# Performance work log

Measured on AMD Instinct MI355X. Metric: run time of the kernel, lower is better.

## Reference

```python
import jax, jax.numpy as jnp
import numpy as np

B, C, H, W = 8, 256, 128, 128
SH, SW = 8, 8            # stoken_size
HH, WW = H // SH, W // SW
NH = 8                   # num_heads
HD = C // NH             # head_dim = 32
KD = HD                  # key_dim (attn_ratio=1)
ATTN_SCALE = KD ** (-0.5)
AFF_SCALE = C ** (-0.5)


def unfold9(x):
    """x: (B,C,hh,ww) -> (B, hh*ww, C, 9); matches Unfold(3) + transpose/reshape."""
    b, c, hh, ww = x.shape
    xp = jnp.pad(x, ((0, 0), (0, 0), (1, 1), (1, 1)))
    p = jnp.stack([xp[:, :, dy:dy + hh, dx:dx + ww]
                   for dy in range(3) for dx in range(3)], axis=2)  # (B,C,9,hh,ww)
    return p.transpose(0, 3, 4, 1, 2).reshape(b, hh * ww, c, 9)


def fold9(y):
    """y: (B,C,9,hh,ww) -> (B,C,hh,ww); matches Fold(3) (conv_transpose with identity kernels)."""
    hh, ww = y.shape[-2:]
    yp = jnp.pad(y, ((0, 0), (0, 0), (0, 0), (1, 1), (1, 1)))
    out = 0.
    for dy in range(3):
        for dx in range(3):
            out = out + yp[:, :, dy * 3 + dx, 2 - dy:2 - dy + hh, 2 - dx:2 - dx + ww]
    return out


def attention(sf, w_qkv, w_pe, w_proj):
    """Attention module with attn_ratio=1 (Conv layers have act=False, BN identity)."""
    b, c, hh, ww = sf.shape
    n = hh * ww
    qkv = jnp.einsum('oc,bchw->bohw', w_qkv, sf).reshape(b, NH, 2 * KD + HD, n)
    q, k, v = jnp.split(qkv, [KD, 2 * KD], axis=2)
    attn = jax.nn.softmax(jnp.einsum('bhkn,bhkm->bhnm', q, k) * ATTN_SCALE, axis=-1)
    o = jnp.einsum('bhdm,bhnm->bhdn', v, attn).reshape(b, c, hh, ww)
    pe = jax.lax.conv_general_dilated(
        v.reshape(b, c, hh, ww), w_pe, (1, 1), ((1, 1), (1, 1)),
        dimension_numbers=('NCHW', 'OIHW', 'NCHW'), feature_group_count=c)
    return jnp.einsum('oc,bchw->bohw', w_proj, o + pe)


def setup_inputs() -> dict:
    key = jax.random.key(0)
    k0, k1, k2, k3 = jax.random.split(key, 4)
    x = jax.random.normal(k0, (B, C, H, W), dtype=jnp.float32)
    w_qkv = jax.random.normal(k1, (3 * C, C), dtype=jnp.float32) * 0.05
    w_pe = jax.random.normal(k2, (C, 1, 3, 3), dtype=jnp.float32) * 0.05
    w_proj = jax.random.normal(k3, (C, C), dtype=jnp.float32) * 0.05
    return {'x': x, 'w_qkv': w_qkv, 'w_pe': w_pe, 'w_proj': w_proj}


def reference(x, w_qkv, w_pe, w_proj):
    # H,W divisible by stoken_size -> no padding branch
    xb = x.reshape(B, C, HH, SH, WW, SW)
    stoken = xb.mean(axis=(3, 5))                                   # (B,C,hh,ww) adaptive_avg_pool2d
    pix = xb.transpose(0, 2, 4, 3, 5, 1).reshape(B, HH * WW, SH * SW, C)
    # --- single no-grad iteration (n_iter=1) ---
    sf9 = unfold9(stoken)                                            # (B,n,C,9)
    aff = jax.nn.softmax(jnp.einsum('bnpc,bnck->bnpk', pix, sf9) * AFF_SCALE, axis=-1)
    aff = jax.lax.stop_gradient(aff)                                 # torch.no_grad
    asum = aff.sum(axis=2).transpose(0, 2, 1).reshape(B, 1, 9, HH, WW)
    asum = jax.lax.stop_gradient(fold9(asum))                        # (B,1,hh,ww)
    # --- super-token aggregation ---
    sf = jnp.einsum('bnpc,bnpk->bnck', pix, aff)                     # (B,n,C,9)
    sf = fold9(sf.transpose(0, 2, 3, 1).reshape(B, C, 9, HH, WW))    # (B,C,hh,ww)
    sf = sf / (asum + 1e-12)
    # --- refine with attention ---
    sf = attention(sf, w_qkv, w_pe, w_proj)
    # --- scatter back to pixels ---
    sf9b = unfold9(sf)                                               # (B,n,C,9)
    pix_out = jnp.einsum('bnck,bnpk->bnpc', sf9b, aff)               # (B,n,h*w,C)
    return pix_out.reshape(B, HH, WW, C, SH, SW).transpose(0, 3, 1, 4, 2, 5).reshape(B, C, H, W)
```

## Files before the change

### kernel.cpp

```cpp
#include <hip/hip_runtime.h>
#include <cstdint>
#include <cstddef>


#define AFF_SCALE 0.0625f
#define ATTN_SCALE 0.17677669529663687f

__device__ __forceinline__ float dpp_add_xor1(float v) {
    int p = __builtin_amdgcn_update_dpp(0, __float_as_int(v), 0xB1, 0xF, 0xF, true);
    return v + __int_as_float(p);
}
__device__ __forceinline__ float dpp_add_xor2(float v) {
    int p = __builtin_amdgcn_update_dpp(0, __float_as_int(v), 0x4E, 0xF, 0xF, true);
    return v + __int_as_float(p);
}

__global__ __launch_bounds__(128) void stoken_kernel(
    const float* __restrict__ x, float* __restrict__ stok_pad)
{
    int blk = blockIdx.x;
    int i  = blk & 15;
    int bc = blk >> 4;
    int t  = threadIdx.x;
    const float* xr = x + ((size_t)bc * 128 + i * 8) * 128 + t;
    float s = 0.f;
#pragma unroll
    for (int r = 0; r < 8; ++r) s += xr[r * 128];
    s += __shfl_down(s, 4, 64);
    s += __shfl_down(s, 2, 64);
    s += __shfl_down(s, 1, 64);
    if ((t & 7) == 0) {
        int j = t >> 3;
        int b = bc >> 8, c = bc & 255;
        stok_pad[(((size_t)b * 18 + (i + 1)) * 18 + (j + 1)) * 256 + c] =
            s * (1.f / 64.f);
    }
}

__global__ __launch_bounds__(256, 4) void aff_kernel(
    const float* __restrict__ x, const float* __restrict__ stok_pad,
    float* __restrict__ aff_g, float* __restrict__ asum_g)
{
    __shared__ __align__(16) float sfs[9 * 260];
    __shared__ __align__(16) float part[576];

    int bid  = blockIdx.x;
    int xcd  = bid & 7, slot_ = bid >> 3;
    int pair = xcd * 128 + (slot_ >> 1);
    int m = pair & 7, i = (pair >> 3) & 15, b = pair >> 7;
    int j = m * 2 + (slot_ & 1);
    int bn = b * 256 + i * 16 + j;
    int t = threadIdx.x;

    {
        const float* spT = stok_pad + (size_t)b * 324 * 256;
#pragma unroll
        for (int dy = 0; dy < 3; ++dy)
#pragma unroll
            for (int dx = 0; dx < 3; ++dx) {
                int r = i + dy, cn = j + dx;
                float v = 0.f;
                if ((unsigned)(r - 1) < 16u && (unsigned)(cn - 1) < 16u)
                    v = spT[((size_t)r * 18 + cn) * 256 + t];
                sfs[(dy * 3 + dx) * 260 + t] = v;
            }
    }
    part[t] = 0.f;
    part[t + 256] = 0.f;
    if (t < 64) part[t + 512] = 0.f;
    __syncthreads();

    int w = t >> 6, l = t & 63;
    {
        int pq = l >> 2, cgl = l & 3;
        int cbase = w * 64 + cgl * 16;
        int pi = pq >> 1, pj4 = (pq & 1) * 4;
        const float* xb = x + (size_t)(b * 256) * 16384
                            + (size_t)(i * 8 + pi) * 128 + j * 8 + pj4;
        float acc[4][9];
#pragma unroll
        for (int ii = 0; ii < 4; ++ii)
#pragma unroll
            for (int k = 0; k < 9; ++k) acc[ii][k] = 0.f;

#pragma unroll
        for (int c4i = 0; c4i < 4; ++c4i) {
            int c = cbase + c4i * 4;
            const float4 p0 = *(const float4*)&xb[(size_t)(c + 0) * 16384];
            const float4 p1 = *(const float4*)&xb[(size_t)(c + 1) * 16384];
            const float4 p2 = *(const float4*)&xb[(size_t)(c + 2) * 16384];
            const float4 p3 = *(const float4*)&xb[(size_t)(c + 3) * 16384];
#pragma unroll
            for (int k = 0; k < 9; ++k) {
                const float4 sv = *(const float4*)&sfs[k * 260 + c];
                acc[0][k] += p0.x * sv.x + p1.x * sv.y + p2.x * sv.z + p3.x * sv.w;
                acc[1][k] += p0.y * sv.x + p1.y * sv.y + p2.y * sv.z + p3.y * sv.w;
                acc[2][k] += p0.z * sv.x + p1.z * sv.y + p2.z * sv.z + p3.z * sv.w;
                acc[3][k] += p0.w * sv.x + p1.w * sv.y + p2.w * sv.z + p3.w * sv.w;
            }
        }
#pragma unroll
        for (int ii = 0; ii < 4; ++ii)
#pragma unroll
            for (int k = 0; k < 9; ++k) {
                acc[ii][k] = dpp_add_xor1(acc[ii][k]);
                acc[ii][k] = dpp_add_xor2(acc[ii][k]);
            }
#pragma unroll
        for (int k = 0; k < 9; ++k) {
            float v01 = (cgl & 1) ? acc[1][k] : acc[0][k];
            float v23 = (cgl & 1) ? acc[3][k] : acc[2][k];
            float vk  = (cgl & 2) ? v23 : v01;
            atomicAdd(&part[l * 9 + k], vk);
        }
    }
    __syncthreads();

    if (t < 64) {
        float a[9];
        float mx = -1e30f;
#pragma unroll
        for (int k = 0; k < 9; ++k) {
            float v = part[t * 9 + k] * AFF_SCALE;
            a[k] = v;
            mx = fmaxf(mx, v);
        }
        float ssum = 0.f;
#pragma unroll
        for (int k = 0; k < 9; ++k) { a[k] = __expf(a[k] - mx); ssum += a[k]; }
        float inv = 1.f / ssum;
#pragma unroll
        for (int k = 0; k < 9; ++k) {
            a[k] *= inv;
            aff_g[(size_t)bn * 576 + k * 64 + t] = a[k];
        }
#pragma unroll
        for (int k = 0; k < 9; ++k) {
            float r = a[k];
            r += __shfl_down(r, 32, 64); r += __shfl_down(r, 16, 64);
            r += __shfl_down(r, 8, 64);  r += __shfl_down(r, 4, 64);
            r += __shfl_down(r, 2, 64);  r += __shfl_down(r, 1, 64);
            if (t == 0) asum_g[(size_t)bn * 9 + k] = r;
        }
    }
}

__global__ __launch_bounds__(256, 4) void agg_kernel(
    const float* __restrict__ x, const float* __restrict__ aff_g,
    float* __restrict__ agg)
{
    __shared__ __align__(16) float affs[9 * 64];

    int bid  = blockIdx.x;
    int xcd  = bid & 7, slot_ = bid >> 3;
    int pair = xcd * 128 + (slot_ >> 1);
    int m = pair & 7, i = (pair >> 3) & 15, b = pair >> 7;
    int j = m * 2 + (slot_ & 1);
    int bn = b * 256 + i * 16 + j;
    int t = threadIdx.x;

    {
        const float* ag = aff_g + (size_t)bn * 576;
        affs[t] = ag[t];
        affs[t + 256] = ag[t + 256];
        if (t < 64) affs[t + 512] = ag[t + 512];
    }
    __syncthreads();

    int w = t >> 6, l = t & 63;
    int cql = l >> 2, pq2 = l & 3;
    int cb2 = w * 64 + cql * 4;
    const float* xb = x + (size_t)(b * 256) * 16384 + (size_t)(i * 8) * 128 + j * 8;
    float acc2[4][9];
#pragma unroll
    for (int ii = 0; ii < 4; ++ii)
#pragma unroll
        for (int k = 0; k < 9; ++k) acc2[ii][k] = 0.f;

#pragma unroll
    for (int pp = 0; pp < 4; ++pp) {
        int p4 = pq2 * 4 + pp;
        int pi = p4 >> 1, pj4 = (p4 & 1) * 4;
        const float* xr = xb + (size_t)pi * 128 + pj4;
        const float4 q0 = *(const float4*)&xr[(size_t)(cb2 + 0) * 16384];
        const float4 q1 = *(const float4*)&xr[(size_t)(cb2 + 1) * 16384];
        const float4 q2 = *(const float4*)&xr[(size_t)(cb2 + 2) * 16384];
        const float4 q3 = *(const float4*)&xr[(size_t)(cb2 + 3) * 16384];
#pragma unroll
        for (int k = 0; k < 9; ++k) {
            const float4 av = *(const float4*)&affs[k * 64 + p4 * 4];
            acc2[0][k] += q0.x * av.x + q0.y * av.y + q0.z * av.z + q0.w * av.w;
            acc2[1][k] += q1.x * av.x + q1.y * av.y + q1.z * av.z + q1.w * av.w;
            acc2[2][k] += q2.x * av.x + q2.y * av.y + q2.z * av.z + q2.w * av.w;
            acc2[3][k] += q3.x * av.x + q3.y * av.y + q3.z * av.z + q3.w * av.w;
        }
    }
#pragma unroll
    for (int ii = 0; ii < 4; ++ii)
#pragma unroll
        for (int k = 0; k < 9; ++k) {
            acc2[ii][k] = dpp_add_xor1(acc2[ii][k]);
            acc2[ii][k] = dpp_add_xor2(acc2[ii][k]);
        }
    int cout = w * 64 + l;
#pragma unroll
    for (int k = 0; k < 9; ++k) {
        float v01 = (pq2 & 1) ? acc2[1][k] : acc2[0][k];
        float v23 = (pq2 & 1) ? acc2[3][k] : acc2[2][k];
        float vk  = (pq2 & 2) ? v23 : v01;
        agg[((size_t)bn * 9 + k) * 256 + cout] = vk;
    }
}

__global__ __launch_bounds__(256) void fold_div_kernel(
    const float* __restrict__ agg, const float* __restrict__ asum_g,
    float* __restrict__ sf)
{
    __shared__ float v[256 * 17];
    int b = blockIdx.x >> 4, y = blockIdx.x & 15;
    int t = threadIdx.x;
    for (int x = 0; x < 16; ++x) {
        float af = 0.f, val = 0.f;
#pragma unroll
        for (int dy = 0; dy < 3; ++dy)
#pragma unroll
            for (int dx = 0; dx < 3; ++dx) {
                int ii = y + 1 - dy, jj = x + 1 - dx;
                if ((unsigned)ii < 16u && (unsigned)jj < 16u) {
                    int idx = (b * 256 + ii * 16 + jj) * 9 + dy * 3 + dx;
                    af  += asum_g[idx];
                    val += agg[(size_t)idx * 256 + t];
                }
            }
        v[t * 17 + x] = val / (af + 1e-12f);
    }
    __syncthreads();
    int xw = t & 15, cw0 = t >> 4;
#pragma unroll
    for (int it = 0; it < 16; ++it) {
        int c = cw0 + it * 16;
        sf[((size_t)b * 256 + c) * 256 + y * 16 + xw] = v[c * 17 + xw];
    }
}

__global__ __launch_bounds__(256) void gemm_w(
    const float* __restrict__ A, const float* __restrict__ Bm,
    float* __restrict__ Cout, int M, int mode)
{
    __shared__ float As[32 * 68];
    __shared__ float Bs[32 * 64];
    int b = blockIdx.x, o0 = blockIdx.y * 64, n0 = blockIdx.z * 64;
    int t = threadIdx.x;
    int tr = t >> 4, tc = t & 15;
    const float* Bb = Bm + (size_t)b * 256 * 256;
    float acc[4][4];
#pragma unroll
    for (int ii = 0; ii < 4; ++ii)
#pragma unroll
        for (int jj = 0; jj < 4; ++jj) acc[ii][jj] = 0.f;

    for (int k0 = 0; k0 < 256; k0 += 32) {
        {
            int ol = t >> 2, kq = (t & 3) * 8;
            const float* Ap = A + (size_t)(o0 + ol) * 256 + k0 + kq;
            const float4 f0 = *(const float4*)&Ap[0];
            const float4 f1 = *(const float4*)&Ap[4];
            As[(kq + 0) * 68 + ol] = f0.x; As[(kq + 1) * 68 + ol] = f0.y;
            As[(kq + 2) * 68 + ol] = f0.z; As[(kq + 3) * 68 + ol] = f0.w;
            As[(kq + 4) * 68 + ol] = f1.x; As[(kq + 5) * 68 + ol] = f1.y;
            As[(kq + 6) * 68 + ol] = f1.z; As[(kq + 7) * 68 + ol] = f1.w;
        }
#pragma unroll
        for (int i2 = 0; i2 < 8; ++i2) {
            int e = t + i2 * 256;
            int kl = e >> 6, nl = e & 63;
            Bs[kl * 64 + nl] = Bb[(size_t)(k0 + kl) * 256 + n0 + nl];
        }
        __syncthreads();
#pragma unroll
        for (int kk = 0; kk < 32; ++kk) {
            const float4 av = *(const float4*)&As[kk * 68 + tr * 4];
            const float4 bv = *(const float4*)&Bs[kk * 64 + tc * 4];
            acc[0][0] += av.x * bv.x; acc[0][1] += av.x * bv.y; acc[0][2] += av.x * bv.z; acc[0][3] += av.x * bv.w;
            acc[1][0] += av.y * bv.x; acc[1][1] += av.y * bv.y; acc[1][2] += av.y * bv.z; acc[1][3] += av.y * bv.w;
            acc[2][0] += av.z * bv.x; acc[2][1] += av.z * bv.y; acc[2][2] += av.z * bv.z; acc[2][3] += av.z * bv.w;
            acc[3][0] += av.w * bv.x; acc[3][1] += av.w * bv.y; acc[3][2] += av.w * bv.z; acc[3][3] += av.w * bv.w;
        }
        __syncthreads();
    }

    if (mode == 0) {
#pragma unroll
        for (int ii = 0; ii < 4; ++ii) {
            int o = o0 + tr * 4 + ii;
            float4 st = make_float4(acc[ii][0], acc[ii][1], acc[ii][2], acc[ii][3]);
            *(float4*)&Cout[((size_t)b * M + o) * 256 + n0 + tc * 4] = st;
        }
    } else {
#pragma unroll
        for (int jj = 0; jj < 4; ++jj) {
            int n = n0 + tc * 4 + jj;
            int y = n >> 4, x = n & 15;
            float4 st = make_float4(acc[0][jj], acc[1][jj], acc[2][jj], acc[3][jj]);
            *(float4*)&Cout[(((size_t)b * 18 + 1 + y) * 18 + 1 + x) * 256 + o0 + tr * 4] = st;
        }
    }
}

__global__ __launch_bounds__(256) void attn_kernel(
    const float* __restrict__ qkv, float* __restrict__ o_attn)
{
    __shared__ float smem[9216];
    int b = blockIdx.x, h = blockIdx.y, nt = blockIdx.z;
    int t = threadIdx.x, nl = t & 63, mq = t >> 6;
    int n = nt * 64 + nl;

    {
        int dd = t >> 3, mb = (t & 7) * 32;
        const float* krow = qkv + ((size_t)b * 768 + h * 96 + 32 + dd) * 256;
#pragma unroll
        for (int e4 = 0; e4 < 8; ++e4) {
            int m = mb + e4 * 4;
            const float4 kw = *(const float4*)&krow[m];
            smem[(m + 0) * 32 + dd] = kw.x; smem[(m + 1) * 32 + dd] = kw.y;
            smem[(m + 2) * 32 + dd] = kw.z; smem[(m + 3) * 32 + dd] = kw.w;
        }
    }
    float q[32];
    {
        const float* qbase = qkv + ((size_t)b * 768 + h * 96) * 256 + n;
#pragma unroll
        for (int d = 0; d < 32; ++d) q[d] = qbase[(size_t)d * 256];
    }
    __syncthreads();

    float l[64];
#pragma unroll
    for (int e = 0; e < 64; ++e) {
        const float* kp = &smem[(mq * 64 + e) * 32];
        float s = 0.f;
#pragma unroll
        for (int d4 = 0; d4 < 8; ++d4) {
            const float4 kv4 = *(const float4*)&kp[d4 * 4];
            s += q[d4 * 4 + 0] * kv4.x + q[d4 * 4 + 1] * kv4.y +
                 q[d4 * 4 + 2] * kv4.z + q[d4 * 4 + 3] * kv4.w;
        }
        l[e] = s * ATTN_SCALE;
    }
    float mx = -1e30f;
#pragma unroll
    for (int e = 0; e < 64; ++e) mx = fmaxf(mx, l[e]);
    float sm = 0.f;
#pragma unroll
    for (int e = 0; e < 64; ++e) { l[e] = __expf(l[e] - mx); sm += l[e]; }
    __syncthreads();

    {
        int dd = t >> 3, mb = (t & 7) * 32;
        const float* vrow = qkv + ((size_t)b * 768 + h * 96 + 64 + dd) * 256;
#pragma unroll
        for (int e4 = 0; e4 < 8; ++e4) {
            int m = mb + e4 * 4;
            const float4 vw = *(const float4*)&vrow[m];
            smem[(m + 0) * 32 + dd] = vw.x; smem[(m + 1) * 32 + dd] = vw.y;
            smem[(m + 2) * 32 + dd] = vw.z; smem[(m + 3) * 32 + dd] = vw.w;
        }
    }
    __syncthreads();

    float oa[32];
#pragma unroll
    for (int d = 0; d < 32; ++d) oa[d] = 0.f;
#pragma unroll
    for (int e = 0; e < 64; ++e) {
        float pm = l[e];
        const float* vp = &smem[(mq * 64 + e) * 32];
#pragma unroll
        for (int d4 = 0; d4 < 8; ++d4) {
            const float4 vv = *(const float4*)&vp[d4 * 4];
            oa[d4 * 4 + 0] += pm * vv.x; oa[d4 * 4 + 1] += pm * vv.y;
            oa[d4 * 4 + 2] += pm * vv.z; oa[d4 * 4 + 3] += pm * vv.w;
        }
    }
    __syncthreads();

    float* op   = smem;
    float* mxsm = smem + 8448;
    {
        int idx = mq * 64 + nl;
#pragma unroll
        for (int d = 0; d < 32; ++d) op[idx * 33 + d] = oa[d];
        mxsm[idx * 2 + 0] = mx;
        mxsm[idx * 2 + 1] = sm;
    }
    __syncthreads();

    if (t < 64) {
        float M2 = -1e30f;
#pragma unroll
        for (int q4 = 0; q4 < 4; ++q4) M2 = fmaxf(M2, mxsm[(q4 * 64 + t) * 2]);
        float w[4], S = 0.f;
#pragma unroll
        for (int q4 = 0; q4 < 4; ++q4) {
            w[q4] = __expf(mxsm[(q4 * 64 + t) * 2] - M2);
            S += mxsm[(q4 * 64 + t) * 2 + 1] * w[q4];
        }
        float inv = 1.f / S;
#pragma unroll
        for (int d = 0; d < 32; ++d) {
            float o = 0.f;
#pragma unroll
            for (int q4 = 0; q4 < 4; ++q4) o += op[(q4 * 64 + t) * 33 + d] * w[q4];
            o_attn[((size_t)b * 256 + h * 32 + d) * 256 + nt * 64 + t] = o * inv;
        }
    }
}

__global__ __launch_bounds__(256) void peadd_kernel(
    const float* __restrict__ qkv, const float* __restrict__ w_pe,
    float* __restrict__ o_attn)
{
    int bc = blockIdx.x;
    int b = bc >> 8, c = bc & 255;
    int t = threadIdx.x;
    int y = t >> 4, x = t & 15;
    int h = c >> 5, d = c & 31;
    const float* v = qkv + ((size_t)b * 768 + h * 96 + 64 + d) * 256;
    float acc = o_attn[(size_t)bc * 256 + t];
#pragma unroll
    for (int ky = 0; ky < 3; ++ky)
#pragma unroll
        for (int kx = 0; kx < 3; ++kx) {
            int yy = y + ky - 1, xx = x + kx - 1;
            if ((unsigned)yy < 16u && (unsigned)xx < 16u)
                acc += w_pe[c * 9 + ky * 3 + kx] * v[yy * 16 + xx];
        }
    o_attn[(size_t)bc * 256 + t] = acc;
}

__global__ __launch_bounds__(256) void scatter_kernel(
    const float* __restrict__ sfa_pad, const float* __restrict__ aff_g,
    float* __restrict__ out)
{
    __shared__ float ss[3 * 18 * 40];
    __shared__ float aff_s[16 * 577];

    int blk = blockIdx.x;
    int pi = blk & 7, i = (blk >> 3) & 15, b = blk >> 7;
    int t = threadIdx.x;

    for (int e = t; e < 1728; e += 256) {
        int dy = e / 576, rem = e % 576;
        int col = rem >> 5, idx = rem & 31;
        int q = idx >> 3, d = idx & 7;
        int row = i + dy;
        float v = 0.f;
        if ((unsigned)(row - 1) < 16u && (unsigned)(col - 1) < 16u)
            v = sfa_pad[(((size_t)b * 18 + row) * 18 + col) * 256 + q * 64 + pi * 8 + d];
        ss[(dy * 18 + col) * 40 + idx] = v;
    }
    {
        const float* ag = aff_g + ((size_t)b * 256 + i * 16) * 576;
        for (int e = t; e < 9216; e += 256) {
            int j = e / 576, rem = e % 576;
            int k = rem >> 6, p = rem & 63;
            aff_s[j * 577 + p * 9 + k] = ag[j * 576 + rem];
        }
    }
    __syncthreads();

    int lane = t & 63, w = t >> 6;
    int j0 = lane >> 3, pj = lane & 7;
    int j1 = j0 + 8;

    float S0[4][9], S1[4][9];
#pragma unroll
    for (int q = 0; q < 4; ++q)
#pragma unroll
        for (int k = 0; k < 9; ++k) {
            int dy = k / 3, dx = k % 3;
            S0[q][k] = ss[(dy * 18 + j0 + dx) * 40 + q * 8 + pj];
            S1[q][k] = ss[(dy * 18 + j1 + dx) * 40 + q * 8 + pj];
        }

    int y = i * 8 + pi;
    size_t ob = (size_t)b * 256 * 16384 + (size_t)y * 128;
    const float* A0 = &aff_s[j0 * 577];
    const float* A1 = &aff_s[j1 * 577];
    for (int p = w * 16; p < w * 16 + 16; ++p) {
        float a0[9], a1[9];
#pragma unroll
        for (int k = 0; k < 9; ++k) { a0[k] = A0[p * 9 + k]; a1[k] = A1[p * 9 + k]; }
#pragma unroll
        for (int q = 0; q < 4; ++q) {
            int c2 = p * 4 + q;
            float v0 = 0.f, v1 = 0.f;
#pragma unroll
            for (int k = 0; k < 9; ++k) {
                v0 += S0[q][k] * a0[k];
                v1 += S1[q][k] * a1[k];
            }
            out[ob + (size_t)c2 * 16384 + lane] = v0;
            out[ob + (size_t)c2 * 16384 + 64 + lane] = v1;
        }
    }
}

extern "C" void kernel_launch(void* const* d_in, const int* in_sizes, int n_in,
                              void* d_out, int out_size, void* d_ws, size_t ws_size,
                              hipStream_t stream) {
    const float* x      = (const float*)d_in[0];
    const float* w_qkv  = (const float*)d_in[1];
    const float* w_pe   = (const float*)d_in[2];
    const float* w_proj = (const float*)d_in[3];
    float* out = (float*)d_out;
    float* agg = (float*)d_out;

    float* ws = (float*)d_ws;
    const size_t o_aff  = 0;
    const size_t o_asum = 1179648;
    const size_t o_pad  = 1198080;
    const size_t o_sf   = 1861632;
    const size_t o_qkv  = 2385920;

    stoken_kernel<<<8 * 256 * 16, 128, 0, stream>>>(x, ws + o_pad);
    aff_kernel<<<8 * 256, 256, 0, stream>>>(x, ws + o_pad, ws + o_aff, ws + o_asum);
    agg_kernel<<<8 * 256, 256, 0, stream>>>(x, ws + o_aff, agg);
    fold_div_kernel<<<8 * 16, 256, 0, stream>>>(agg, ws + o_asum, ws + o_sf);
    gemm_w<<<dim3(8, 12, 4), 256, 0, stream>>>(w_qkv, ws + o_sf, ws + o_qkv, 768, 0);
    attn_kernel<<<dim3(8, 8, 4), 256, 0, stream>>>(ws + o_qkv, ws + o_sf);
    peadd_kernel<<<8 * 256, 256, 0, stream>>>(ws + o_qkv, w_pe, ws + o_sf);
    gemm_w<<<dim3(8, 4, 4), 256, 0, stream>>>(w_proj, ws + o_sf, ws + o_pad, 256, 1);
    scatter_kernel<<<8 * 16 * 8, 256, 0, stream>>>(ws + o_pad, ws + o_aff, out);
}
```

Measured before the change: 442.1 us.

## Fuse affinity and aggregation kernels, split attention and proj GEMM for more blocks

Merges the affinity softmax and the aggregation pass into one kernel, so the affinities stay in shared memory and neither a reload of aff from global memory nor a separate launch is needed. The attention kernel now gives each block 32 queries instead of 64, with 8 key-chunks merged per query, doubling the grid. The projection GEMM moves to a dedicated 32-row-tile kernel that writes straight into the padded layout, doubling its block count. The fused kernel keeps both phases' registers live in one launch, which may lower occupancy.

```diff
diff --git a/kernel.cpp b/kernel.cpp
--- a/kernel.cpp
+++ b/kernel.cpp
@@ -37,12 +37,14 @@
     }
 }
 
-__global__ __launch_bounds__(256, 4) void aff_kernel(
+__global__ __launch_bounds__(256, 4) void aff_agg_kernel(
     const float* __restrict__ x, const float* __restrict__ stok_pad,
-    float* __restrict__ aff_g, float* __restrict__ asum_g)
+    float* __restrict__ aff_g, float* __restrict__ asum_g,
+    float* __restrict__ agg)
 {
     __shared__ __align__(16) float sfs[9 * 260];
     __shared__ __align__(16) float part[576];
+    __shared__ __align__(16) float affs[576];
 
     int bid  = blockIdx.x;
     int xcd  = bid & 7, slot_ = bid >> 3;
@@ -71,6 +73,7 @@
     __syncthreads();
 
     int w = t >> 6, l = t & 63;
+
     {
         int pq = l >> 2, cgl = l & 3;
         int cbase = w * 64 + cgl * 16;
@@ -132,6 +135,7 @@
 #pragma unroll
         for (int k = 0; k < 9; ++k) {
             a[k] *= inv;
+            affs[k * 64 + t] = a[k];
             aff_g[(size_t)bn * 576 + k * 64 + t] = a[k];
         }
 #pragma unroll
@@ -143,72 +147,51 @@
             if (t == 0) asum_g[(size_t)bn * 9 + k] = r;
         }
     }
-}
-
-__global__ __launch_bounds__(256, 4) void agg_kernel(
-    const float* __restrict__ x, const float* __restrict__ aff_g,
-    float* __restrict__ agg)
-{
-    __shared__ __align__(16) float affs[9 * 64];
-
-    int bid  = blockIdx.x;
-    int xcd  = bid & 7, slot_ = bid >> 3;
-    int pair = xcd * 128 + (slot_ >> 1);
-    int m = pair & 7, i = (pair >> 3) & 15, b = pair >> 7;
-    int j = m * 2 + (slot_ & 1);
-    int bn = b * 256 + i * 16 + j;
-    int t = threadIdx.x;
-
-    {
-        const float* ag = aff_g + (size_t)bn * 576;
-        affs[t] = ag[t];
-        affs[t + 256] = ag[t + 256];
-        if (t < 64) affs[t + 512] = ag[t + 512];
-    }
-    __syncthreads();
-
-    int w = t >> 6, l = t & 63;
-    int cql = l >> 2, pq2 = l & 3;
-    int cb2 = w * 64 + cql * 4;
-    const float* xb = x + (size_t)(b * 256) * 16384 + (size_t)(i * 8) * 128 + j * 8;
-    float acc2[4][9];
-#pragma unroll
-    for (int ii = 0; ii < 4; ++ii)
-#pragma unroll
-        for (int k = 0; k < 9; ++k) acc2[ii][k] = 0.f;
-
-#pragma unroll
-    for (int pp = 0; pp < 4; ++pp) {
-        int p4 = pq2 * 4 + pp;
-        int pi = p4 >> 1, pj4 = (p4 & 1) * 4;
-        const float* xr = xb + (size_t)pi * 128 + pj4;
-        const float4 q0 = *(const float4*)&xr[(size_t)(cb2 + 0) * 16384];
-        const float4 q1 = *(const float4*)&xr[(size_t)(cb2 + 1) * 16384];
-        const float4 q2 = *(const float4*)&xr[(size_t)(cb2 + 2) * 16384];
-        const float4 q3 = *(const float4*)&xr[(size_t)(cb2 + 3) * 16384];
+    __syncthreads();
+
+    {
+        int cql = l >> 2, pq2 = l & 3;
+        int cb2 = w * 64 + cql * 4;
+        const float* xb = x + (size_t)(b * 256) * 16384 + (size_t)(i * 8) * 128 + j * 8;
+        float acc2[4][9];
+#pragma unroll
+        for (int ii = 0; ii < 4; ++ii)
+#pragma unroll
+            for (int k = 0; k < 9; ++k) acc2[ii][k] = 0.f;
+
+#pragma unroll
+        for (int pp = 0; pp < 4; ++pp) {
+            int p4 = pq2 * 4 + pp;
+            int pi = p4 >> 1, pj4 = (p4 & 1) * 4;
+            const float* xr = xb + (size_t)pi * 128 + pj4;
+            const float4 q0 = *(const float4*)&xr[(size_t)(cb2 + 0) * 16384];
+            const float4 q1 = *(const float4*)&xr[(size_t)(cb2 + 1) * 16384];
+            const float4 q2 = *(const float4*)&xr[(size_t)(cb2 + 2) * 16384];
+            const float4 q3 = *(const float4*)&xr[(size_t)(cb2 + 3) * 16384];
+#pragma unroll
+            for (int k = 0; k < 9; ++k) {
+                const float4 av = *(const float4*)&affs[k * 64 + p4 * 4];
+                acc2[0][k] += q0.x * av.x + q0.y * av.y + q0.z * av.z + q0.w * av.w;
+                acc2[1][k] += q1.x * av.x + q1.y * av.y + q1.z * av.z + q1.w * av.w;
+                acc2[2][k] += q2.x * av.x + q2.y * av.y + q2.z * av.z + q2.w * av.w;
+                acc2[3][k] += q3.x * av.x + q3.y * av.y + q3.z * av.z + q3.w * av.w;
+            }
+        }
+#pragma unroll
+        for (int ii = 0; ii < 4; ++ii)
+#pragma unroll
+            for (int k = 0; k < 9; ++k) {
+                acc2[ii][k] = dpp_add_xor1(acc2[ii][k]);
+                acc2[ii][k] = dpp_add_xor2(acc2[ii][k]);
+            }
+        int cout = w * 64 + l;
 #pragma unroll
         for (int k = 0; k < 9; ++k) {
-            const float4 av = *(const float4*)&affs[k * 64 + p4 * 4];
-            acc2[0][k] += q0.x * av.x + q0.y * av.y + q0.z * av.z + q0.w * av.w;
-            acc2[1][k] += q1.x * av.x + q1.y * av.y + q1.z * av.z + q1.w * av.w;
-            acc2[2][k] += q2.x * av.x + q2.y * av.y + q2.z * av.z + q2.w * av.w;
-            acc2[3][k] += q3.x * av.x + q3.y * av.y + q3.z * av.z + q3.w * av.w;
-        }
-    }
-#pragma unroll
-    for (int ii = 0; ii < 4; ++ii)
-#pragma unroll
-        for (int k = 0; k < 9; ++k) {
-            acc2[ii][k] = dpp_add_xor1(acc2[ii][k]);
-            acc2[ii][k] = dpp_add_xor2(acc2[ii][k]);
-        }
-    int cout = w * 64 + l;
-#pragma unroll
-    for (int k = 0; k < 9; ++k) {
-        float v01 = (pq2 & 1) ? acc2[1][k] : acc2[0][k];
-        float v23 = (pq2 & 1) ? acc2[3][k] : acc2[2][k];
-        float vk  = (pq2 & 2) ? v23 : v01;
-        agg[((size_t)bn * 9 + k) * 256 + cout] = vk;
+            float v01 = (pq2 & 1) ? acc2[1][k] : acc2[0][k];
+            float v23 = (pq2 & 1) ? acc2[3][k] : acc2[2][k];
+            float vk  = (pq2 & 2) ? v23 : v01;
+            agg[((size_t)bn * 9 + k) * 256 + cout] = vk;
+        }
     }
 }
 
@@ -245,7 +228,7 @@
 
 __global__ __launch_bounds__(256) void gemm_w(
     const float* __restrict__ A, const float* __restrict__ Bm,
-    float* __restrict__ Cout, int M, int mode)
+    float* __restrict__ Cout, int M)
 {
     __shared__ float As[32 * 68];
     __shared__ float Bs[32 * 64];
@@ -289,21 +272,63 @@
         __syncthreads();
     }
 
-    if (mode == 0) {
-#pragma unroll
-        for (int ii = 0; ii < 4; ++ii) {
-            int o = o0 + tr * 4 + ii;
-            float4 st = make_float4(acc[ii][0], acc[ii][1], acc[ii][2], acc[ii][3]);
-            *(float4*)&Cout[((size_t)b * M + o) * 256 + n0 + tc * 4] = st;
-        }
-    } else {
-#pragma unroll
-        for (int jj = 0; jj < 4; ++jj) {
-            int n = n0 + tc * 4 + jj;
-            int y = n >> 4, x = n & 15;
-            float4 st = make_float4(acc[0][jj], acc[1][jj], acc[2][jj], acc[3][jj]);
-            *(float4*)&Cout[(((size_t)b * 18 + 1 + y) * 18 + 1 + x) * 256 + o0 + tr * 4] = st;
-        }
+#pragma unroll
+    for (int ii = 0; ii < 4; ++ii) {
+        int o = o0 + tr * 4 + ii;
+        float4 st = make_float4(acc[ii][0], acc[ii][1], acc[ii][2], acc[ii][3]);
+        *(float4*)&Cout[((size_t)b * M + o) * 256 + n0 + tc * 4] = st;
+    }
+}
+
+__global__ __launch_bounds__(256) void gemm_proj32(
+    const float* __restrict__ A, const float* __restrict__ Bm,
+    float* __restrict__ Cout)
+{
+    __shared__ float As[32 * 36];
+    __shared__ float Bs[32 * 64];
+    int b = blockIdx.x, o0 = blockIdx.y * 32, n0 = blockIdx.z * 64;
+    int t = threadIdx.x;
+    int tr = t >> 4, tc = t & 15;
+    const float* Bb = Bm + (size_t)b * 256 * 256;
+    float acc[2][4];
+#pragma unroll
+    for (int ii = 0; ii < 2; ++ii)
+#pragma unroll
+        for (int jj = 0; jj < 4; ++jj) acc[ii][jj] = 0.f;
+
+    for (int k0 = 0; k0 < 256; k0 += 32) {
+        {
+            int ol = t & 31, kq = (t >> 5) * 4;
+            const float* Ap = A + (size_t)(o0 + ol) * 256 + k0 + kq;
+            const float4 f = *(const float4*)&Ap[0];
+            As[(kq + 0) * 36 + ol] = f.x; As[(kq + 1) * 36 + ol] = f.y;
+            As[(kq + 2) * 36 + ol] = f.z; As[(kq + 3) * 36 + ol] = f.w;
+        }
+#pragma unroll
+        for (int i2 = 0; i2 < 8; ++i2) {
+            int e = t + i2 * 256;
+            int kl = e >> 6, nl = e & 63;
+            Bs[kl * 64 + nl] = Bb[(size_t)(k0 + kl) * 256 + n0 + nl];
+        }
+        __syncthreads();
+#pragma unroll
+        for (int kk = 0; kk < 32; ++kk) {
+            const float2 av = *(const float2*)&As[kk * 36 + tr * 2];
+            const float4 bv = *(const float4*)&Bs[kk * 64 + tc * 4];
+            acc[0][0] += av.x * bv.x; acc[0][1] += av.x * bv.y;
+            acc[0][2] += av.x * bv.z; acc[0][3] += av.x * bv.w;
+            acc[1][0] += av.y * bv.x; acc[1][1] += av.y * bv.y;
+            acc[1][2] += av.y * bv.z; acc[1][3] += av.y * bv.w;
+        }
+        __syncthreads();
+    }
+
+#pragma unroll
+    for (int jj = 0; jj < 4; ++jj) {
+        int n = n0 + tc * 4 + jj;
+        int y = n >> 4, x = n & 15;
+        float2 st = make_float2(acc[0][jj], acc[1][jj]);
+        *(float2*)&Cout[(((size_t)b * 18 + 1 + y) * 18 + 1 + x) * 256 + o0 + tr * 2] = st;
     }
 }
 
@@ -312,8 +337,8 @@
 {
     __shared__ float smem[9216];
     int b = blockIdx.x, h = blockIdx.y, nt = blockIdx.z;
-    int t = threadIdx.x, nl = t & 63, mq = t >> 6;
-    int n = nt * 64 + nl;
+    int t = threadIdx.x, nl = t & 31, mq = t >> 5;
+    int n = nt * 32 + nl;
 
     {
         int dd = t >> 3, mb = (t & 7) * 32;
@@ -334,10 +359,10 @@
     }
     __syncthreads();
 
-    float l[64];
-#pragma unroll
-    for (int e = 0; e < 64; ++e) {
-        const float* kp = &smem[(mq * 64 + e) * 32];
+    float l[32];
+#pragma unroll
+    for (int e = 0; e < 32; ++e) {
+        const float* kp = &smem[(mq * 32 + e) * 32];
         float s = 0.f;
 #pragma unroll
         for (int d4 = 0; d4 < 8; ++d4) {
@@ -349,10 +374,10 @@
     }
     float mx = -1e30f;
 #pragma unroll
-    for (int e = 0; e < 64; ++e) mx = fmaxf(mx, l[e]);
+    for (int e = 0; e < 32; ++e) mx = fmaxf(mx, l[e]);
     float sm = 0.f;
 #pragma unroll
-    for (int e = 0; e < 64; ++e) { l[e] = __expf(l[e] - mx); sm += l[e]; }
+    for (int e = 0; e < 32; ++e) { l[e] = __expf(l[e] - mx); sm += l[e]; }
     __syncthreads();
 
     {
@@ -372,9 +397,9 @@
 #pragma unroll
     for (int d = 0; d < 32; ++d) oa[d] = 0.f;
 #pragma unroll
-    for (int e = 0; e < 64; ++e) {
+    for (int e = 0; e < 32; ++e) {
         float pm = l[e];
-        const float* vp = &smem[(mq * 64 + e) * 32];
+        const float* vp = &smem[(mq * 32 + e) * 32];
 #pragma unroll
         for (int d4 = 0; d4 < 8; ++d4) {
             const float4 vv = *(const float4*)&vp[d4 * 4];
@@ -387,7 +412,7 @@
     float* op   = smem;
     float* mxsm = smem + 8448;
     {
-        int idx = mq * 64 + nl;
+        int idx = mq * 32 + nl;
 #pragma unroll
         for (int d = 0; d < 32; ++d) op[idx * 33 + d] = oa[d];
         mxsm[idx * 2 + 0] = mx;
@@ -395,23 +420,23 @@
     }
     __syncthreads();
 
-    if (t < 64) {
+    if (t < 32) {
         float M2 = -1e30f;
 #pragma unroll
-        for (int q4 = 0; q4 < 4; ++q4) M2 = fmaxf(M2, mxsm[(q4 * 64 + t) * 2]);
-        float w[4], S = 0.f;
-#pragma unroll
-        for (int q4 = 0; q4 < 4; ++q4) {
-            w[q4] = __expf(mxsm[(q4 * 64 + t) * 2] - M2);
-            S += mxsm[(q4 * 64 + t) * 2 + 1] * w[q4];
+        for (int q8 = 0; q8 < 8; ++q8) M2 = fmaxf(M2, mxsm[(q8 * 32 + t) * 2]);
+        float w[8], S = 0.f;
+#pragma unroll
+        for (int q8 = 0; q8 < 8; ++q8) {
+            w[q8] = __expf(mxsm[(q8 * 32 + t) * 2] - M2);
+            S += mxsm[(q8 * 32 + t) * 2 + 1] * w[q8];
         }
         float inv = 1.f / S;
 #pragma unroll
         for (int d = 0; d < 32; ++d) {
             float o = 0.f;
 #pragma unroll
-            for (int q4 = 0; q4 < 4; ++q4) o += op[(q4 * 64 + t) * 33 + d] * w[q4];
-            o_attn[((size_t)b * 256 + h * 32 + d) * 256 + nt * 64 + t] = o * inv;
+            for (int q8 = 0; q8 < 8; ++q8) o += op[(q8 * 32 + t) * 33 + d] * w[q8];
+            o_attn[((size_t)b * 256 + h * 32 + d) * 256 + nt * 32 + t] = o * inv;
         }
     }
 }
@@ -524,12 +549,12 @@
     const size_t o_qkv  = 2385920;
 
     stoken_kernel<<<8 * 256 * 16, 128, 0, stream>>>(x, ws + o_pad);
-    aff_kernel<<<8 * 256, 256, 0, stream>>>(x, ws + o_pad, ws + o_aff, ws + o_asum);
-    agg_kernel<<<8 * 256, 256, 0, stream>>>(x, ws + o_aff, agg);
+    aff_agg_kernel<<<8 * 256, 256, 0, stream>>>(x, ws + o_pad, ws + o_aff,
+                                                ws + o_asum, agg);
     fold_div_kernel<<<8 * 16, 256, 0, stream>>>(agg, ws + o_asum, ws + o_sf);
-    gemm_w<<<dim3(8, 12, 4), 256, 0, stream>>>(w_qkv, ws + o_sf, ws + o_qkv, 768, 0);
-    attn_kernel<<<dim3(8, 8, 4), 256, 0, stream>>>(ws + o_qkv, ws + o_sf);
+    gemm_w<<<dim3(8, 12, 4), 256, 0, stream>>>(w_qkv, ws + o_sf, ws + o_qkv, 768);
+    attn_kernel<<<dim3(8, 8, 8), 256, 0, stream>>>(ws + o_qkv, ws + o_sf);
     peadd_kernel<<<8 * 256, 256, 0, stream>>>(ws + o_qkv, w_pe, ws + o_sf);
-    gemm_w<<<dim3(8, 4, 4), 256, 0, stream>>>(w_proj, ws + o_sf, ws + o_pad, 256, 1);
+    gemm_proj32<<<dim3(8, 8, 4), 256, 0, stream>>>(w_proj, ws + o_sf, ws + o_pad);
     scatter_kernel<<<8 * 16 * 8, 256, 0, stream>>>(ws + o_pad, ws + o_aff, out);
 }
```

Measured after the change: 434.6 us. Within noise of the previous version (-1.7%).
